# Performance work log

Hardware: AMD Instinct MI355X
Metric: run time of the kernel (lower is better)

Reference implementation:

```python
import jax, jax.numpy as jnp
import numpy as np

D = 192
HEADS = 4
HD = D // HEADS
R = 3  # correlation radius actually used in forward_level
NDISP = (2 * R + 1) ** 2  # 49
T = 3  # frames -> 2 consecutive pairs
ITERS = 4


def layer_norm(x, w, b, eps=1e-5):
    m = jnp.mean(x, axis=-1, keepdims=True)
    v = jnp.var(x, axis=-1, keepdims=True)
    return (x - m) / jnp.sqrt(v + eps) * w + b


def mha(x, in_w, in_b, out_w, out_b):
    # torch nn.MultiheadAttention, batch_first, self-attention
    B, N, _ = x.shape
    qkv = x @ in_w.T + in_b
    q, k, v = jnp.split(qkv, 3, axis=-1)
    q = q.reshape(B, N, HEADS, HD).transpose(0, 2, 1, 3) * (1.0 / float(np.sqrt(HD)))
    k = k.reshape(B, N, HEADS, HD).transpose(0, 2, 1, 3)
    v = v.reshape(B, N, HEADS, HD).transpose(0, 2, 1, 3)
    att = jax.nn.softmax(jnp.einsum('bhqd,bhkd->bhqk', q, k), axis=-1)
    y = jnp.einsum('bhqk,bhkd->bhqd', att, v).transpose(0, 2, 1, 3).reshape(B, N, D)
    return y @ out_w.T + out_b


def tblock(x, p):
    ln1w, ln1b, inw, inb, ow, ob, ln2w, ln2b, w1, b1, w2, b2 = p
    x = x + mha(layer_norm(x, ln1w, ln1b), inw, inb, ow, ob)
    h = layer_norm(x, ln2w, ln2b)
    h = jax.nn.gelu(h @ w1.T + b1, approximate=False) @ w2.T + b2
    return x + h


def local_corr(f1, f2):
    C = f1.shape[1]
    scale = 1.0 / float(np.sqrt(C))
    outs = []
    for dy in range(-R, R + 1):
        for dx in range(-R, R + 1):
            f2s = jnp.roll(f2, (dy, dx), axis=(2, 3))
            outs.append(jnp.sum(f1 * f2s, axis=1) * scale)
    return jnp.stack(outs, axis=1)


def grid_sample_bilinear_border(img, grid):
    # img: B,C,H,W; grid: B,Ho,Wo,2 with (x,y) in [-1,1]; align_corners=True, border padding
    B, C, H, W = img.shape
    x = jnp.clip((grid[..., 0] + 1.0) * 0.5 * (W - 1), 0.0, W - 1)
    y = jnp.clip((grid[..., 1] + 1.0) * 0.5 * (H - 1), 0.0, H - 1)
    x0 = jnp.floor(x); y0 = jnp.floor(y)
    x1 = jnp.minimum(x0 + 1, W - 1); y1 = jnp.minimum(y0 + 1, H - 1)
    wx = (x - x0)[:, None]; wy = (y - y0)[:, None]
    imgf = img.reshape(B, C, H * W)
    Ho, Wo = x.shape[1], x.shape[2]
    def gather(yy, xx):
        idx = (yy * W + xx).astype(jnp.int32).reshape(B, 1, Ho * Wo)
        return jnp.take_along_axis(imgf, idx, axis=2).reshape(B, C, Ho, Wo)
    v00 = gather(y0, x0); v01 = gather(y0, x1)
    v10 = gather(y1, x0); v11 = gather(y1, x1)
    return v00 * (1 - wx) * (1 - wy) + v01 * wx * (1 - wy) + v10 * (1 - wx) * wy + v11 * wx * wy


def warp(img, flow):
    # flow in pixels, Bx2xHxW
    B, C, H, W = img.shape
    xs = jnp.linspace(-1.0, 1.0, W); ys = jnp.linspace(-1.0, 1.0, H)
    gx, gy = jnp.meshgrid(xs, ys)  # each (H, W), 'xy' indexing
    base = jnp.stack([gx, gy], axis=-1)[None]
    off = jnp.stack([flow[:, 0] * (2.0 / max(W - 1, 1)),
                     flow[:, 1] * (2.0 / max(H - 1, 1))], axis=-1)
    return grid_sample_bilinear_border(img, base + off)


def upsample2x_align(img):
    # F.interpolate(scale_factor=2, mode='bilinear', align_corners=True)
    B, C, H, W = img.shape
    Ho, Wo = 2 * H, 2 * W
    xs = jnp.linspace(-1.0, 1.0, Wo); ys = jnp.linspace(-1.0, 1.0, Ho)
    gx, gy = jnp.meshgrid(xs, ys)
    grid = jnp.broadcast_to(jnp.stack([gx, gy], axis=-1)[None], (B, Ho, Wo, 2))
    return grid_sample_bilinear_border(img, grid)


def conv2d(x, w, b):
    y = jax.lax.conv_general_dilated(x, w, (1, 1), ((1, 1), (1, 1)),
                                     dimension_numbers=('NCHW', 'OIHW', 'NCHW'))
    return y + b[None, :, None, None]


def _forward(feats_l1, feats_l2, feats_l3, tok_w, tok_b,
             lcm_ln1_w, lcm_ln1_b, lcm_in_w, lcm_in_b, lcm_out_w, lcm_out_b,
             lcm_ln2_w, lcm_ln2_b, lcm_mlp_w1, lcm_mlp_b1, lcm_mlp_w2, lcm_mlp_b2,
             gtr_ln1_w, gtr_ln1_b, gtr_in_w, gtr_in_b, gtr_out_w, gtr_out_b,
             gtr_ln2_w, gtr_ln2_b, gtr_mlp_w1, gtr_mlp_b1, gtr_mlp_w2, gtr_mlp_b2,
             head_w1, head_b1, head_w2, head_b2,
             ref1_w1, ref1_b1, ref1_w2, ref1_b2,
             ref0_w1, ref0_b1, ref0_w2, ref0_b2):
    feats = [[feats_l1[t] for t in range(T)],
             [feats_l2[t] for t in range(T)],
             [feats_l3[t] for t in range(T)]]
    # ---- CostTokenizer ----
    tokens = []
    for lvl in range(3):
        toks = []
        for k in range(T - 1):
            corr = local_corr(feats[lvl][k], feats[lvl][k + 1])
            toks.append(jnp.einsum('bchw,dc->bdhw', corr, tok_w[lvl]) + tok_b[lvl][None, :, None, None])
        tokens.append(toks)
    lcm_p = [(lcm_ln1_w[i], lcm_ln1_b[i], lcm_in_w[i], lcm_in_b[i], lcm_out_w[i], lcm_out_b[i],
              lcm_ln2_w[i], lcm_ln2_b[i], lcm_mlp_w1[i], lcm_mlp_b1[i], lcm_mlp_w2[i], lcm_mlp_b2[i])
             for i in range(lcm_ln1_w.shape[0])]
    gtr_p = [(gtr_ln1_w[i], gtr_ln1_b[i], gtr_in_w[i], gtr_in_b[i], gtr_out_w[i], gtr_out_b[i],
              gtr_ln2_w[i], gtr_ln2_b[i], gtr_mlp_w1[i], gtr_mlp_b1[i], gtr_mlp_w2[i], gtr_mlp_b2[i])
             for i in range(gtr_ln1_w.shape[0])]
    # ---- LatentCostMemory (EMA state; .detach() -> stop_gradient; state resets when N changes) ----
    state = None
    latent = []
    for toks in tokens:
        lvl_lat = []
        for tok in toks:
            B_, Dd, H, W = tok.shape
            x = tok.reshape(B_, Dd, H * W).transpose(0, 2, 1)  # b (h w) d
            for p in lcm_p:
                x = tblock(x, p)
            if state is None or state.shape[1] != x.shape[1]:
                state = jax.lax.stop_gradient(x)
            x = 0.8 * x + 0.2 * state
            state = jax.lax.stop_gradient(x)
            lvl_lat.append(x.transpose(0, 2, 1))  # b d n
        latent.append(lvl_lat)
    H8, W8 = feats[1][0].shape[-2:]
    coarse = []
    for lat in latent[1]:
        x = lat.transpose(0, 2, 1)
        for p in gtr_p:
            x = tblock(x, p)
        fv = jax.nn.gelu(x @ head_w1.T + head_b1, approximate=False) @ head_w2.T + head_b2
        coarse.append(fv.transpose(0, 2, 1).reshape(-1, 2, H8, W8))
    # ---- MSRecurrentDecoder ----
    outs = []
    for k, f8 in enumerate(coarse):
        cur = f8
        for _ in range(ITERS):
            w10 = warp(feats[1][k + 1], cur)
            x = jnp.concatenate([feats[1][k], cur, w10], axis=1)
            cur = cur + conv2d(jax.nn.gelu(conv2d(x, ref1_w1, ref1_b1), approximate=False), ref1_w2, ref1_b2)
        cur2 = upsample2x_align(cur)
        for _ in range(ITERS):
            w10 = warp(feats[0][k + 1], cur2)
            x = jnp.concatenate([feats[0][k], cur2, w10], axis=1)
            cur2 = cur2 + conv2d(jax.nn.gelu(conv2d(x, ref0_w1, ref0_b1), approximate=False), ref0_w2, ref0_b2)
        outs.append(cur2)
    return jnp.stack(outs)  # [pairs, B, 2, H/4, W/4]


def setup_inputs():
    key = jax.random.key(0)
    ks = iter(jax.random.split(key, 64))
    def rn(shape, s=1.0):
        return jax.random.normal(next(ks), shape, dtype=jnp.float32) * s
    B = 1
    inp = {}
    inp['feats_l1'] = rn((T, B, 64, 64, 64))
    inp['feats_l2'] = rn((T, B, 128, 32, 32))
    inp['feats_l3'] = rn((T, B, 192, 16, 16))
    inp['tok_w'] = rn((3, D, NDISP), 0.02)
    inp['tok_b'] = rn((3, D), 0.02)
    for pre, n in (('lcm', 6), ('gtr', 2)):
        inp[pre + '_ln1_w'] = jnp.ones((n, D), jnp.float32)
        inp[pre + '_ln1_b'] = jnp.zeros((n, D), jnp.float32)
        inp[pre + '_in_w'] = rn((n, 3 * D, D), 0.02)
        inp[pre + '_in_b'] = rn((n, 3 * D), 0.02)
        inp[pre + '_out_w'] = rn((n, D, D), 0.02)
        inp[pre + '_out_b'] = rn((n, D), 0.02)
        inp[pre + '_ln2_w'] = jnp.ones((n, D), jnp.float32)
        inp[pre + '_ln2_b'] = jnp.zeros((n, D), jnp.float32)
        inp[pre + '_mlp_w1'] = rn((n, 4 * D, D), 0.02)
        inp[pre + '_mlp_b1'] = rn((n, 4 * D), 0.02)
        inp[pre + '_mlp_w2'] = rn((n, D, 4 * D), 0.02)
        inp[pre + '_mlp_b2'] = rn((n, D), 0.02)
    inp['head_w1'] = rn((D, D), 0.02); inp['head_b1'] = rn((D,), 0.02)
    inp['head_w2'] = rn((2, D), 0.02); inp['head_b2'] = rn((2,), 0.02)
    inp['ref1_w1'] = rn((128, 258, 3, 3), 0.02); inp['ref1_b1'] = rn((128,), 0.02)
    inp['ref1_w2'] = rn((2, 128, 3, 3), 0.02); inp['ref1_b2'] = rn((2,), 0.02)
    inp['ref0_w1'] = rn((64, 130, 3, 3), 0.02); inp['ref0_b1'] = rn((64,), 0.02)
    inp['ref0_w2'] = rn((2, 64, 3, 3), 0.02); inp['ref0_b2'] = rn((2,), 0.02)
    return inp


def reference(feats_l1, feats_l2, feats_l3, tok_w, tok_b,
              lcm_ln1_w, lcm_ln1_b, lcm_in_w, lcm_in_b, lcm_out_w, lcm_out_b,
              lcm_ln2_w, lcm_ln2_b, lcm_mlp_w1, lcm_mlp_b1, lcm_mlp_w2, lcm_mlp_b2,
              gtr_ln1_w, gtr_ln1_b, gtr_in_w, gtr_in_b, gtr_out_w, gtr_out_b,
              gtr_ln2_w, gtr_ln2_b, gtr_mlp_w1, gtr_mlp_b1, gtr_mlp_w2, gtr_mlp_b2,
              head_w1, head_b1, head_w2, head_b2,
              ref1_w1, ref1_b1, ref1_w2, ref1_b2,
              ref0_w1, ref0_b1, ref0_w2, ref0_b2):
    return _forward(feats_l1, feats_l2, feats_l3, tok_w, tok_b,
                    lcm_ln1_w, lcm_ln1_b, lcm_in_w, lcm_in_b, lcm_out_w, lcm_out_b,
                    lcm_ln2_w, lcm_ln2_b, lcm_mlp_w1, lcm_mlp_b1, lcm_mlp_w2, lcm_mlp_b2,
                    gtr_ln1_w, gtr_ln1_b, gtr_in_w, gtr_in_b, gtr_out_w, gtr_out_b,
                    gtr_ln2_w, gtr_ln2_b, gtr_mlp_w1, gtr_mlp_b1, gtr_mlp_w2, gtr_mlp_b2,
                    head_w1, head_b1, head_w2, head_b2,
                    ref1_w1, ref1_b1, ref1_w2, ref1_b2,
                    ref0_w1, ref0_b1, ref0_w2, ref0_b2)
```

## Files before the change

### kernel.cpp

```cpp
#include <hip/hip_runtime.h>
#include <hip/hip_bf16.h>

typedef __hip_bfloat16 bf16;
typedef short bf16x8 __attribute__((ext_vector_type(8)));
typedef float f32x4 __attribute__((ext_vector_type(4)));

#define DEV __device__ __forceinline__

DEV float bf2f(bf16 v) { return __bfloat162float(v); }
DEV bf16 f2bf(float v) { return __float2bfloat16(v); }
DEV unsigned short bfr(float f) {
  bf16 h = __float2bfloat16(f);
  return *reinterpret_cast<unsigned short*>(&h);
}
DEV float shf(unsigned short u) {
  unsigned int x = ((unsigned int)u) << 16;
  return *reinterpret_cast<float*>(&x);
}
DEV float gelu_exact(float x) { return 0.5f * x * (1.0f + erff(x * 0.70710678118654752f)); }

DEV float ldw(const void* p, long i, int isb) {
  return isb ? __bfloat162float(((const bf16*)p)[i]) : ((const float*)p)[i];
}

// ... 40 lines not shown
  if (i >= n) return;
  int s = i / (NP * ICP);
  int r = i - s * NP * ICP;
  int oc = r / ICP, icp = r - oc * ICP;
  float v = 0.0f;
  if (oc < OC) {
    int ic = -1;
    if (icp < C) ic = icp;
    else if (icp < 2 * C) ic = icp - C + C + 2;
    else if (icp < 2 * C + 2) ic = icp - 2 * C + C;
    if (ic >= 0 && ic < ICT) v = ldw(src, ((long)oc * ICT + ic) * 9 + s, isb);
  }
  dst[i] = f2bf(v);
}

__global__ void k_trans_feats(const void* __restrict__ in, bf16* __restrict__ Fp,
                              int F, int C, int HW, const int* __restrict__ fl) {
  int isb = *fl;
  int cpg = C >> 3;
  int n = F * HW * cpg;
  int i = blockIdx.x * blockDim.x + threadIdx.x;
  if (i >= n) return;
  int p = i % HW;
  int rem = i / HW;
  int c8 = rem % cpg;
  int f = rem / cpg;
  long base = (long)f * C * HW + (long)(c8 * 8) * HW + p;
  union { unsigned short u[8]; uint4 v; } pk;
#pragma unroll
  for (int j = 0; j < 8; ++j) pk.u[j] = bfr(ldw(in, base + (long)j * HW, isb));
  *(uint4*)((unsigned short*)Fp + ((long)f * HW + p) * C + c8 * 8) = pk.v;
}

__global__ void k_fill_feats(const bf16* __restrict__ Fp, bf16* __restrict__ Ap,
                             int C, int ICP, int H, int W) {
  int HW = H * W;
  int cpg = C >> 3;
  int n = 2 * HW * cpg;
  int i = blockIdx.x * blockDim.x + threadIdx.x;
  if (i >= n) return;
  int g = i % cpg;
  int rem = i / cpg;
  int p = rem % HW;
  int b = rem / HW;
  int h = p / W, w = p - h * W;
  const unsigned short* src = (const unsigned short*)Fp + ((long)b * HW + p) * C + g * 8;
  unsigned short* dst = (unsigned short*)Ap +
      ((long)b * (H + 2) * (W + 2) + (long)(h + 1) * (W + 2) + w + 1) * ICP + g * 8;
  *(uint4*)dst = *(const uint4*)src;
}

__global__ void k_warp_pack(const bf16* __restrict__ Fp, const float* __restrict__ flow,
                            bf16* __restrict__ Ap, int C, int ICP, int H, int W) {
  int HW = H * W;
  int cpg = C >> 3;
  int n = 2 * HW * cpg;
  int i = blockIdx.x * blockDim.x + threadIdx.x;
  if (i >= n) return;
  int g = i % cpg;
  int rem = i / cpg;
  int p = rem % HW;
  int b = rem / HW;
  int h = p / W, w = p - h * W;
  const float* fl = flow + (long)b * 2 * HW;
  float fx = fl[p], fy = fl[HW + p];
  unsigned short* drow = (unsigned short*)Ap +
      ((long)b * (H + 2) * (W + 2) + (long)(h + 1) * (W + 2) + w + 1) * ICP;
  if (g == 0) { drow[2 * C] = bfr(fx); drow[2 * C + 1] = bfr(fy); }
  float x = fminf(fmaxf((float)w + fx, 0.0f), (float)(W - 1));
  float y = fminf(fmaxf((float)h + fy, 0.0f), (float)(H - 1));
  int x0 = (int)floorf(x), y0 = (int)floorf(y);
  int x1 = min(x0 + 1, W - 1), y1 = min(y0 + 1, H - 1);
  float wx = x - (float)x0, wy = y - (float)y0;
  float w00 = (1 - wx) * (1 - wy), w01 = wx * (1 - wy);
  float w10 = (1 - wx) * wy, w11 = wx * wy;
  const unsigned short* f = (const unsigned short*)Fp + (long)(b + 1) * HW * C;
  int c = g * 8;
  union { unsigned short u[8]; uint4 v; } a = { .v = *(const uint4*)(f + (long)(y0 * W + x0) * C + c) };
  union { unsigned short u[8]; uint4 v; } bb = { .v = *(const uint4*)(f + (long)(y0 * W + x1) * C + c) };
  union { unsigned short u[8]; uint4 v; } cc = { .v = *(const uint4*)(f + (long)(y1 * W + x0) * C + c) };
  union { unsigned short u[8]; uint4 v; } dd = { .v = *(const uint4*)(f + (long)(y1 * W + x1) * C + c) };
  union { unsigned short u[8]; uint4 v; } o;
#pragma unroll
  for (int j = 0; j < 8; ++j) {
    float v = shf(a.u[j]) * w00 + shf(bb.u[j]) * w01 + shf(cc.u[j]) * w10 + shf(dd.u[j]) * w11;
    o.u[j] = bfr(v);
  }
  *(uint4*)(drow + C + c) = o.v;
}

template <int MW, int NT, int MODE>
__global__ __launch_bounds__(256) void k_conv_mfma(
    const bf16* __restrict__ Ap, int ICP, const bf16* __restrict__ Wp,
    const float* __restrict__ bias, const float* __restrict__ res,
    void* __restrict__ out, int NOUT, int H, int W, int lgW) {
  constexpr int NWN = 4 / MW;
  constexpr int BM = MW * 16;
  constexpr int BN = NWN * NT * 16;
  __shared__ unsigned short Asm[198][40];
  __shared__ unsigned short Wsm[9 * BN][40];
  int tid = threadIdx.x;
  int wv = tid >> 6, ln = tid & 63, quad = ln >> 4, l16 = ln & 15;
  int wm = wv % MW, wn = wv / MW;
  int n0 = blockIdx.x * BN;
  int m0 = blockIdx.y * BM;
  int b = blockIdx.z;
  int Wp2 = W + 2;
  int CW = (BM < W) ? BM : W;
  int lgCW = (CW == 64) ? 6 : 5;
  int RO = (BM > W) ? (BM >> lgW) : 1;
  int ACW = CW + 2;
  int AR = (RO + 2) * ACW;
  int py0 = m0 >> lgW;
  int px0 = m0 & (W - 1);
  const unsigned short* A = (const unsigned short*)Ap + (long)b * (H + 2) * Wp2 * ICP;
  int NPr = (MODE == 0) ? NOUT : 16;
  int nk = ICP >> 5;
  f32x4 acc[NT] = {};
  int mm_local = wm * 16 + l16;
  int plr = mm_local >> lgCW;
  int plc = mm_local & (CW - 1);
// ... 49 lines not shown
        ((float*)out)[(long)b * 2 * HW + (long)n * HW + mmo] = v;
      }
    }
  }
}

__global__ void k_corr(const bf16* __restrict__ Fp2, bf16* __restrict__ corrT) {
  __shared__ unsigned short f1r[128];
  int p = blockIdx.x;
  int b = blockIdx.y;
  int t = threadIdx.x;
  const unsigned short* f1 = (const unsigned short*)Fp2 + ((long)b * 1024 + p) * 128;
  if (t < 16) *(uint4*)&f1r[t * 8] = *(const uint4*)(f1 + t * 8);
  __syncthreads();
  long rowo = ((long)b * 1024 + p) * 64;
  if (t < 49) {
    int dy = t / 7 - 3, dx = t % 7 - 3;
    int h = p >> 5, w = p & 31;
    int p2 = (((h - dy) & 31) << 5) | ((w - dx) & 31);
    const unsigned short* f2 = (const unsigned short*)Fp2 + ((long)(b + 1) * 1024 + p2) * 128;
    float s = 0.0f;
    for (int c = 0; c < 128; c += 8) {
      union { unsigned short u[8]; uint4 v; } av = { .v = *(const uint4*)&f1r[c] };
      union { unsigned short u[8]; uint4 v; } bv = { .v = *(const uint4*)(f2 + c) };
#pragma unroll
      for (int j = 0; j < 8; ++j) s += shf(av.u[j]) * shf(bv.u[j]);
    }
    corrT[rowo + t] = f2bf(s * 0.08838834764831845f);
  } else {
    corrT[rowo + t] = f2bf(0.0f);
  }
}

template <int KT, int ACT, bool HASRES, int AMODE, int OUTBF, int VT>
__global__ __launch_bounds__(256) void k_gemm_mfma2(
    const void* __restrict__ A, const void* __restrict__ W, long woff,
    const void* __restrict__ bias, long boff, const int* __restrict__ flb,
    const float* __restrict__ res, void* __restrict__ C,
    int M, int N, const int* __restrict__ fl,
    const unsigned short* __restrict__ mop, const float* __restrict__ mml,
    bf16* __restrict__ vtout,
    const void* __restrict__ lnw, long lnwoff,
    const void* __restrict__ lnb, long lnboff) {
  (void)M;
  int isb = *fl;
  __shared__ unsigned short Asm[6][64][40];
  __shared__ unsigned short Wsm[6][64][40];
  int tid = threadIdx.x;
  int wv = tid >> 6, ln = tid & 63;
  int quad = ln >> 4, l16 = ln & 15;
  int m0 = blockIdx.y * 64, n0 = blockIdx.x * 64;
  f32x4 acc[4] = {};
  constexpr int NKC = ((KT < 192) ? KT : 192) >> 5;
  for (int s0 = 0; s0 < KT; s0 += 192) {
    if (s0) __syncthreads();
    for (int i = tid; i < NKC * 256; i += 256) {
      int c4 = i & 3, r = (i >> 2) & 63, kc = i >> 8;
      long eo = woff + (long)(n0 + r) * KT + s0 + kc * 32 + c4 * 8;
      if (isb) {
        *(uint4*)&Wsm[kc][r][c4 * 8] = *(const uint4*)((const unsigned short*)W + eo);
      } else {
        const float* wp = (const float*)W + eo;
        float4 w0 = *(const float4*)wp;
        float4 w1 = *(const float4*)(wp + 4);
        union { unsigned short u[8]; uint4 v; } pk;
        pk.u[0] = bfr(w0.x); pk.u[1] = bfr(w0.y); pk.u[2] = bfr(w0.z); pk.u[3] = bfr(w0.w);
        pk.u[4] = bfr(w1.x); pk.u[5] = bfr(w1.y); pk.u[6] = bfr(w1.z); pk.u[7] = bfr(w1.w);
        *(uint4*)&Wsm[kc][r][c4 * 8] = pk.v;
      }
    }
    if constexpr (AMODE == 1) {
      for (int i = tid; i < NKC * 256; i += 256) {
        int c4 = i & 3, r = (i >> 2) & 63, kc = i >> 8;
        const unsigned short* ap =
            (const unsigned short*)A + (long)(m0 + r) * KT + s0 + kc * 32 + c4 * 8;
        *(uint4*)&Asm[kc][r][c4 * 8] = *(const uint4*)ap;
      }
    } else if constexpr (AMODE == 0) {
      for (int i = tid; i < NKC * 256; i += 256) {
        int c4 = i & 3, r = (i >> 2) & 63, kc = i >> 8;
        const float* ap = (const float*)A + (long)(m0 + r) * KT + s0 + kc * 32 + c4 * 8;
        float4 a0 = *(const float4*)ap;
        float4 a1 = *(const float4*)(ap + 4);
        union { unsigned short u[8]; uint4 v; } pk;
        pk.u[0] = bfr(a0.x); pk.u[1] = bfr(a0.y); pk.u[2] = bfr(a0.z); pk.u[3] = bfr(a0.w);
        pk.u[4] = bfr(a1.x); pk.u[5] = bfr(a1.y); pk.u[6] = bfr(a1.z); pk.u[7] = bfr(a1.w);
        *(uint4*)&Asm[kc][r][c4 * 8] = pk.v;
      }
    } else if constexpr (AMODE == 3) {
      int row = tid >> 2, j = tid & 3;
      const float* xr = (const float*)A + (long)(m0 + row) * 192 + j * 8;
      float av[48];
#pragma unroll
      for (int kc = 0; kc < 6; ++kc) {
        float4 v0 = *(const float4*)(xr + kc * 32);
        float4 v1 = *(const float4*)(xr + kc * 32 + 4);
        av[kc * 8 + 0] = v0.x; av[kc * 8 + 1] = v0.y;
        av[kc * 8 + 2] = v0.z; av[kc * 8 + 3] = v0.w;
        av[kc * 8 + 4] = v1.x; av[kc * 8 + 5] = v1.y;
        av[kc * 8 + 6] = v1.z; av[kc * 8 + 7] = v1.w;
      }
      float sum = 0.0f;
#pragma unroll
      for (int q = 0; q < 48; ++q) sum += av[q];
      sum += __shfl_xor(sum, 1);
      sum += __shfl_xor(sum, 2);
      float mean = sum * (1.0f / 192.0f);
      float vs = 0.0f;
#pragma unroll
      for (int q = 0; q < 48; ++q) { float d = av[q] - mean; vs += d * d; }
      vs += __shfl_xor(vs, 1);
      vs += __shfl_xor(vs, 2);
      float rstd = rsqrtf(vs * (1.0f / 192.0f) + 1e-5f);
#pragma unroll
      for (int kc = 0; kc < 6; ++kc) {
        union { unsigned short u[8]; uint4 v; } pk;
#pragma unroll
        for (int e = 0; e < 8; ++e) {
          long k = kc * 32 + j * 8 + e;
          float g = ldw(lnw, lnwoff + k, isb);
          float bb = ldw(lnb, lnboff + k, isb);
          pk.u[e] = bfr((av[kc * 8 + e] - mean) * rstd * g + bb);
        }
        *(uint4*)&Asm[kc][row][j * 8] = pk.v;
      }
    } else {
      int row = tid >> 2, j = tid & 3;
      int m = m0 + row;
      int rr = m & 1023, bb = m >> 10;
#pragma unroll
      for (int kc = 0; kc < 6; ++kc) {
        int k = kc * 32 + j * 8;
        int h = k / 48;
        int d0 = k - h * 48;
        long idx[4];
        float ms[4], ls[4];
        float Ms = -1e30f;
#pragma unroll
        for (int s = 0; s < 4; ++s) {
          idx[s] = (((long)s * 2 + bb) * 4 + h) * 1024 + rr;
          ms[s] = mml[idx[s] * 2];
          ls[s] = mml[idx[s] * 2 + 1];
          Ms = fmaxf(Ms, ms[s]);
        }
        float e[4], L = 0.0f;
#pragma unroll
        for (int s = 0; s < 4; ++s) { e[s] = __expf(ms[s] - Ms); L += ls[s] * e[s]; }
        float invL = 1.0f / L;
        union { unsigned short u[8]; uint4 v; } pk;
#pragma unroll
        for (int e2 = 0; e2 < 8; ++e2) {
          float o = 0.0f;
#pragma unroll
          for (int s = 0; s < 4; ++s) o += shf(mop[idx[s] * 48 + d0 + e2]) * e[s];
          pk.u[e2] = bfr(o * invL);
        }
        *(uint4*)&Asm[kc][row][j * 8] = pk.v;
      }
    }
    __syncthreads();
#pragma unroll
    for (int kc = 0; kc < NKC; ++kc) {
      bf16x8 af = *(const bf16x8*)&Asm[kc][wv * 16 + l16][quad * 8];
#pragma unroll
      for (int nt = 0; nt < 4; ++nt) {
        bf16x8 wf = *(const bf16x8*)&Wsm[kc][nt * 16 + l16][quad * 8];
        acc[nt] = __builtin_amdgcn_mfma_f32_16x16x32_bf16(af, wf, acc[nt], 0, 0, 0);
      }
    }
  }
  int isbb = *flb;
#pragma unroll
  for (int nt = 0; nt < 4; ++nt) {
    int n = n0 + nt * 16 + l16;
    float bv = ldw(bias, boff + n, isbb);
#pragma unroll
    for (int r = 0; r < 4; ++r) {
      int m = m0 + wv * 16 + quad * 4 + r;
      float v = acc[nt][r] + bv;
      if (HASRES) v += res[(long)m * N + n];
      if (ACT == 1) v = gelu_exact(v);
      if (OUTBF) ((bf16*)C)[(long)m * N + n] = f2bf(v);
      else ((float*)C)[(long)m * N + n] = v;
      if (VT) {
        if (n >= 384) {
          int hh = (n - 384) / 48, dd = (n - 384) % 48;
          int row = m & 1023, bb = m >> 10;
          vtout[((long)(bb * 4 + hh) * 48 + dd) * 1024 + row] = f2bf(v);
        }
      }
    }
  }
}

template <int ACT, bool HASRES, int FLOW>
__global__ __launch_bounds__(256) void k_gemm(const float* __restrict__ A,
                                              const void* __restrict__ W, long woff,
                                              const void* __restrict__ bias, long boff,
                                              const float* __restrict__ res,
                                              float* __restrict__ C, int M, int N, int K, int Kw,
                                              const int* __restrict__ fl) {
  int isb = *fl;
  __shared__ float As[16][132];
  __shared__ float Ws[16][68];
  int tid = threadIdx.x;
  int tx = tid & 15, ty = tid >> 4;
  int m0 = blockIdx.y * 128, n0 = blockIdx.x * 64;
  float acc[8][4] = {};
  for (int k0 = 0; k0 < K; k0 += 16) {
#pragma unroll
    for (int i = 0; i < 2; ++i) {
      int idx4 = tid + i * 256;
      int mm = idx4 >> 2, kc = (idx4 & 3) * 4;
      float4 v = *(const float4*)(A + (long)(m0 + mm) * K + k0 + kc);
      As[kc][mm] = v.x; As[kc + 1][mm] = v.y; As[kc + 2][mm] = v.z; As[kc + 3][mm] = v.w;
    }
#pragma unroll
    for (int i = 0; i < 4; ++i) {
      int idx = tid + i * 256;
      int nn = idx >> 4, kk = idx & 15;
      int gn = n0 + nn, gk = k0 + kk;
      Ws[kk][nn] = (gn < N && gk < Kw) ? ldw(W, woff + (long)gn * Kw + gk, isb) : 0.0f;
    }
    __syncthreads();
#pragma unroll
    for (int kk = 0; kk < 16; ++kk) {
      float4 a0 = *(const float4*)&As[kk][ty * 8];
      float4 a1 = *(const float4*)&As[kk][ty * 8 + 4];
      float4 w4 = *(const float4*)&Ws[kk][tx * 4];
      float av[8] = {a0.x, a0.y, a0.z, a0.w, a1.x, a1.y, a1.z, a1.w};
      float wv[4] = {w4.x, w4.y, w4.z, w4.w};
#pragma unroll
      for (int i = 0; i < 8; ++i)
#pragma unroll
        for (int j = 0; j < 4; ++j) acc[i][j] += av[i] * wv[j];
    }
    __syncthreads();
  }
#pragma unroll
  for (int i = 0; i < 8; ++i) {
    int gm = m0 + ty * 8 + i;
#pragma unroll
    for (int j = 0; j < 4; ++j) {
      int gn = n0 + tx * 4 + j;
      if (gn >= N) continue;
      float v = acc[i][j] + ldw(bias, boff + gn, isb);
      if (HASRES) v += res[(long)gm * N + gn];
      if (ACT == 1) v = gelu_exact(v);
      if (FLOW) {
        int bb2 = gm >> 10, p = gm & 1023;
        C[((long)bb2 * 2 + gn) * 1024 + p] = v;
      } else {
        C[(long)gm * N + gn] = v;
      }
    }
  }
}

__global__ __launch_bounds__(256) void k_attn_mfma(const bf16* __restrict__ qkv,
                                                   const bf16* __restrict__ vt,
                                                   unsigned short* __restrict__ opart,
                                                   float* __restrict__ ml) {
  __shared__ unsigned short Qs[64][72];
  __shared__ unsigned short Ks[64][72];
  __shared__ unsigned short Vs[48][72];
  __shared__ unsigned short Ps[64][72];
  int tid = threadIdx.x;
  int wv = tid >> 6, ln = tid & 63, quad = ln >> 4, l16 = ln & 15;
  int h = blockIdx.y, b = blockIdx.z;
  int qt = blockIdx.x >> 2, s = blockIdx.x & 3;
  int q0 = qt * 64;
  const unsigned short* qp = (const unsigned short*)qkv + (long)b * 1024 * 576;
  const unsigned short* vp = (const unsigned short*)vt + ((long)(b * 4 + h) * 48) * 1024;
  for (int i = tid; i < 384; i += 256) {
    int r = i / 6, c = i % 6;
    *(uint4*)&Qs[r][c * 8] = *(const uint4*)(qp + (long)(q0 + r) * 576 + h * 48 + c * 8);
  }
  for (int i = tid; i < 128; i += 256) {
    int r = i >> 1, c = 6 + (i & 1);
    uint4 z = {0, 0, 0, 0};
    *(uint4*)&Qs[r][c * 8] = z;
  }
  float m[4] = {-1e30f, -1e30f, -1e30f, -1e30f};
  float l[4] = {0.0f, 0.0f, 0.0f, 0.0f};
  f32x4 accO[3] = {};
  const float SC = 0.14433756729740643f;
  for (int kc = s * 4; kc < s * 4 + 4; ++kc) {
    int k0 = kc * 64;
// ... 143 lines not shown
  (void)ws_size; (void)n_in; (void)in_sizes; (void)out_size;

  int* flag = (int*)d_ws;
  int* oneflag = (int*)d_ws + 2;
  float* wsf = (float*)d_ws;
  float* F2   = wsf + 16;
  float* rA   = F2 + 393216;
  float* rX   = rA + 786432;
  float* rT   = rX + 393216;
  float* rY   = rT + 393216;
  float* big  = rY + 393216;
  float* fv   = big + 1572864;
  float* cur  = fv + 4096;
  float* cur2 = cur + 4096;
  float* cb1a = cur2 + 16384;
  float* cb1b = cb1a + 128;
  float* cb0a = cb1b + 16;
  float* cb0b = cb0a + 64;
  bf16* wtok  = (bf16*)(cb0b + 16);
  float* wpk  = cb0b + 16 + 6144;
  bf16* w1p1 = (bf16*)wpk;
  bf16* w1p2 = (bf16*)(wpk + 165888);
  bf16* w0p1 = (bf16*)(wpk + 175104);
  bf16* w0p2 = (bf16*)(wpk + 221184);

  float* x = rX;
  bf16* corrTb = (bf16*)big;
  bf16* qkvbb  = (bf16*)big;
  bf16* vtb    = (bf16*)(big + 655360);
  bf16* hidb   = (bf16*)big;
  unsigned short* opart = (unsigned short*)rA;
  float* mlbuf = rY;
  float* headh = rT;
  bf16* A0p   = (bf16*)rA;
  bf16* A1p   = (bf16*)rX;
  bf16* mid0p = (bf16*)rT;
  bf16* mid1p = (bf16*)rY;
  bf16* Fp2   = (bf16*)(big + 851968);
  bf16* Fp1   = (bf16*)(big + 1048576);

  k_detect<<<1, 256, 0, stream>>>((const unsigned short*)feats_l1, flag);
  k_setone<<<1, 1, 0, stream>>>(oneflag);
  k_cvt<<<1, 256, 0, stream>>>(ref1_b1, cb1a, 128, flag);
  k_cvt<<<1, 256, 0, stream>>>(ref1_b2, cb1b, 2, flag);
  k_cvt<<<1, 256, 0, stream>>>(ref0_b1, cb0a, 64, flag);
  k_cvt<<<1, 256, 0, stream>>>(ref0_b2, cb0b, 2, flag);
  k_padtokw<<<48, 256, 0, stream>>>(tok_w, wtok, flag);
  k_packw<<<1296, 256, 0, stream>>>(ref1_w1, w1p1, 128, 128, 258, 128, 288, 331776, flag);
  k_packw<<<72, 256, 0, stream>>>(ref1_w2, w1p2, 2, 128, 128, 16, 128, 18432, flag);
  k_packw<<<360, 256, 0, stream>>>(ref0_w1, w0p1, 64, 64, 130, 64, 160, 92160, flag);
  k_packw<<<36, 256, 0, stream>>>(ref0_w2, w0p2, 2, 64, 64, 16, 64, 9216, flag);
  k_trans_feats<<<192, 256, 0, stream>>>(feats_l2, Fp2, 3, 128, 1024, flag);
  k_trans_feats<<<384, 256, 0, stream>>>(feats_l1, Fp1, 3, 64, 4096, flag);

  k_corr<<<dim3(1024, 2), 64, 0, stream>>>(Fp2, corrTb);
  k_gemm_mfma2<64, 0, false, 1, 0, 0><<<dim3(3, 32), 256, 0, stream>>>(
      corrTb, wtok, 0, tok_b, 192, flag, nullptr, x, 2048, 192, oneflag,
      nullptr, nullptr, nullptr, nullptr, 0, nullptr, 0);

  auto run_block = [&](const void* ln1w, long o1, const void* ln1b, long o2,
                       const void* inw, long o3, const void* inb, long o4,
                       const void* ow, long o5, const void* ob, long o6,
                       const void* ln2w, long o7, const void* ln2b, long o8,
                       const void* w1, long o9, const void* b1, long o10,
                       const void* w2, long o11, const void* b2, long o12) {
    k_gemm_mfma2<192, 0, false, 3, 1, 1><<<dim3(9, 32), 256, 0, stream>>>(
        x, inw, o3, inb, o4, flag, nullptr, qkvbb, 2048, 576, flag,
        nullptr, nullptr, vtb, ln1w, o1, ln1b, o2);
    k_attn_mfma<<<dim3(64, 4, 2), 256, 0, stream>>>(qkvbb, vtb, opart, mlbuf);
    k_gemm_mfma2<192, 0, true, 2, 0, 0><<<dim3(3, 32), 256, 0, stream>>>(
        nullptr, ow, o5, ob, o6, flag, x, x, 2048, 192, flag,
        opart, mlbuf, nullptr, nullptr, 0, nullptr, 0);
    k_gemm_mfma2<192, 1, false, 3, 1, 0><<<dim3(12, 32), 256, 0, stream>>>(
        x, w1, o9, b1, o10, flag, nullptr, hidb, 2048, 768, flag,
        nullptr, nullptr, nullptr, ln2w, o7, ln2b, o8);
    k_gemm_mfma2<768, 0, true, 1, 0, 0><<<dim3(3, 32), 256, 0, stream>>>(
        hidb, w2, o11, b2, o12, flag, x, x, 2048, 192, flag,
        nullptr, nullptr, nullptr, nullptr, 0, nullptr, 0);
  };

  for (int i = 0; i < 6; ++i) {
    run_block(lcm_ln1_w, (long)i * 192, lcm_ln1_b, (long)i * 192,
              lcm_in_w, (long)i * 110592, lcm_in_b, (long)i * 576,
              lcm_out_w, (long)i * 36864, lcm_out_b, (long)i * 192,
              lcm_ln2_w, (long)i * 192, lcm_ln2_b, (long)i * 192,
              lcm_mlp_w1, (long)i * 147456, lcm_mlp_b1, (long)i * 768,
              lcm_mlp_w2, (long)i * 147456, lcm_mlp_b2, (long)i * 192);
  }
  k_ema<<<768, 256, 0, stream>>>(x);

  for (int i = 0; i < 2; ++i) {
    run_block(gtr_ln1_w, (long)i * 192, gtr_ln1_b, (long)i * 192,
              gtr_in_w, (long)i * 110592, gtr_in_b, (long)i * 576,
              gtr_out_w, (long)i * 36864, gtr_out_b, (long)i * 192,
              gtr_ln2_w, (long)i * 192, gtr_ln2_b, (long)i * 192,
              gtr_mlp_w1, (long)i * 147456, gtr_mlp_b1, (long)i * 768,
              gtr_mlp_w2, (long)i * 147456, gtr_mlp_b2, (long)i * 192);
  }

  k_gemm_mfma2<192, 1, false, 0, 0, 0><<<dim3(3, 32), 256, 0, stream>>>(
      x, head_w1, 0, head_b1, 0, flag, nullptr, headh, 2048, 192, flag,
      nullptr, nullptr, nullptr, nullptr, 0, nullptr, 0);
  k_gemm<0, false, 1><<<dim3(1, 16), 256, 0, stream>>>(headh, head_w2, 0, head_b2, 0, nullptr,
                                                       cur, 2048, 2, 192, 192, flag);

  k_zerosh<<<1920, 256, 0, stream>>>((unsigned short*)rA, 491520);
  k_fill_feats<<<128, 256, 0, stream>>>(Fp2, A1p, 128, 288, 32, 32);

  for (int it = 0; it < 4; ++it) {
    k_warp_pack<<<128, 256, 0, stream>>>(Fp2, cur, A1p, 128, 288, 32, 32);
    k_conv_mfma<2, 2, 0><<<dim3(2, 32, 2), 256, 0, stream>>>(
        A1p, 288, w1p1, cb1a, nullptr, mid1p, 128, 32, 32, 5);
    k_conv_mfma<4, 1, 1><<<dim3(1, 16, 2), 256, 0, stream>>>(
        mid1p, 128, w1p2, cb1b, cur, cur, 2, 32, 32, 5);
  }
  k_upsample<<<64, 256, 0, stream>>>(cur, cur2);
  k_fill_feats<<<256, 256, 0, stream>>>(Fp1, A0p, 64, 160, 64, 64);

  for (int it = 0; it < 4; ++it) {
    k_warp_pack<<<256, 256, 0, stream>>>(Fp1, cur2, A0p, 64, 160, 64, 64);
    k_conv_mfma<2, 2, 0><<<dim3(1, 128, 2), 256, 0, stream>>>(
        A0p, 160, w0p1, cb0a, nullptr, mid0p, 64, 64, 64, 6);
    k_conv_mfma<4, 1, 1><<<dim3(1, 64, 2), 256, 0, stream>>>(
        mid0p, 64, w0p2, cb0b, cur2, cur2, 2, 64, 64, 6);
  }

  k_out<<<64, 256, 0, stream>>>(cur2, d_out, flag);
}
```

Before: 1.087 ms.

## Fuse flow warp and feature packing into first refine conv; tune GEMM tiles

Introduces k_conv_warp, which builds the padded conv input tile in shared memory straight from the features and flow. It does the bilinear warp inline, so the separate fill and warp_pack kernels, their padded staging buffers and most of the zero-fill go away. The MFMA GEMM gains a BM template parameter, and the N=192 GEMMs use 32-row tiles to double the block count. The tiny head projection is moved from a scalar tiled GEMM to a wave-per-output reduction kernel. In exchange, warp work is recomputed for halo pixels and for each output-channel block, and the smaller GEMM tiles reuse weights less.

```diff
diff --git a/kernel.cpp b/kernel.cpp
--- a/kernel.cpp
+++ b/kernel.cpp
@@ -96,61 +96,113 @@
   *(uint4*)((unsigned short*)Fp + ((long)f * HW + p) * C + c8 * 8) = pk.v;
 }
 
-__global__ void k_fill_feats(const bf16* __restrict__ Fp, bf16* __restrict__ Ap,
-                             int C, int ICP, int H, int W) {
+template <int MW, int NT>
+__global__ __launch_bounds__(256) void k_conv_warp(
+    const bf16* __restrict__ Fp, const float* __restrict__ flow, int C, int ICP,
+    const bf16* __restrict__ Wp, const float* __restrict__ bias,
+    void* __restrict__ out, int NOUT, int H, int W, int lgW) {
+  constexpr int NWN = 4 / MW;
+  constexpr int BM = MW * 16;
+  constexpr int BN = NWN * NT * 16;
+  __shared__ unsigned short Asm[102][40];
+  __shared__ unsigned short Wsm[9 * BN][40];
+  int tid = threadIdx.x;
+  int wv = tid >> 6, ln = tid & 63, quad = ln >> 4, l16 = ln & 15;
+  int wm = wv % MW, wn = wv / MW;
+  int n0 = blockIdx.x * BN;
+  int m0 = blockIdx.y * BM;
+  int b = blockIdx.z;
   int HW = H * W;
-  int cpg = C >> 3;
-  int n = 2 * HW * cpg;
-  int i = blockIdx.x * blockDim.x + threadIdx.x;
-  if (i >= n) return;
-  int g = i % cpg;
-  int rem = i / cpg;
-  int p = rem % HW;
-  int b = rem / HW;
-  int h = p / W, w = p - h * W;
-  const unsigned short* src = (const unsigned short*)Fp + ((long)b * HW + p) * C + g * 8;
-  unsigned short* dst = (unsigned short*)Ap +
-      ((long)b * (H + 2) * (W + 2) + (long)(h + 1) * (W + 2) + w + 1) * ICP + g * 8;
-  *(uint4*)dst = *(const uint4*)src;
-}
-
-__global__ void k_warp_pack(const bf16* __restrict__ Fp, const float* __restrict__ flow,
-                            bf16* __restrict__ Ap, int C, int ICP, int H, int W) {
-  int HW = H * W;
-  int cpg = C >> 3;
-  int n = 2 * HW * cpg;
-  int i = blockIdx.x * blockDim.x + threadIdx.x;
-  if (i >= n) return;
-  int g = i % cpg;
-  int rem = i / cpg;
-  int p = rem % HW;
-  int b = rem / HW;
-  int h = p / W, w = p - h * W;
+  int CW = (BM < W) ? BM : W;
+  int lgCW = (CW == 64) ? 6 : 5;
+  int RO = (BM > W) ? (BM >> lgW) : 1;
+  int ACW = CW + 2;
+  int AR = (RO + 2) * ACW;
+  int py0 = m0 >> lgW;
+  int px0 = m0 & (W - 1);
+  const unsigned short* fcur = (const unsigned short*)Fp + (long)b * HW * C;
+  const unsigned short* fnxt = (const unsigned short*)Fp + (long)(b + 1) * HW * C;
   const float* fl = flow + (long)b * 2 * HW;
-  float fx = fl[p], fy = fl[HW + p];
-  unsigned short* drow = (unsigned short*)Ap +
-      ((long)b * (H + 2) * (W + 2) + (long)(h + 1) * (W + 2) + w + 1) * ICP;
-  if (g == 0) { drow[2 * C] = bfr(fx); drow[2 * C + 1] = bfr(fy); }
-  float x = fminf(fmaxf((float)w + fx, 0.0f), (float)(W - 1));
-  float y = fminf(fmaxf((float)h + fy, 0.0f), (float)(H - 1));
-  int x0 = (int)floorf(x), y0 = (int)floorf(y);
-  int x1 = min(x0 + 1, W - 1), y1 = min(y0 + 1, H - 1);
-  float wx = x - (float)x0, wy = y - (float)y0;
-  float w00 = (1 - wx) * (1 - wy), w01 = wx * (1 - wy);
-  float w10 = (1 - wx) * wy, w11 = wx * wy;
-  const unsigned short* f = (const unsigned short*)Fp + (long)(b + 1) * HW * C;
-  int c = g * 8;
-  union { unsigned short u[8]; uint4 v; } a = { .v = *(const uint4*)(f + (long)(y0 * W + x0) * C + c) };
-  union { unsigned short u[8]; uint4 v; } bb = { .v = *(const uint4*)(f + (long)(y0 * W + x1) * C + c) };
-  union { unsigned short u[8]; uint4 v; } cc = { .v = *(const uint4*)(f + (long)(y1 * W + x0) * C + c) };
-  union { unsigned short u[8]; uint4 v; } dd = { .v = *(const uint4*)(f + (long)(y1 * W + x1) * C + c) };
-  union { unsigned short u[8]; uint4 v; } o;
-#pragma unroll
-  for (int j = 0; j < 8; ++j) {
-    float v = shf(a.u[j]) * w00 + shf(bb.u[j]) * w01 + shf(cc.u[j]) * w10 + shf(dd.u[j]) * w11;
-    o.u[j] = bfr(v);
-  }
-  *(uint4*)(drow + C + c) = o.v;
+  int nk = ICP >> 5;
+  f32x4 acc[NT] = {};
+  int mm_local = wm * 16 + l16;
+  int plr = mm_local >> lgCW;
+  int plc = mm_local & (CW - 1);
+  for (int kc = 0; kc < nk; ++kc) {
+    int chbase = kc * 32;
+    for (int i = tid; i < AR * 4; i += 256) {
+      int r = i >> 2, c4 = i & 3;
+      int sr = r / ACW, sc = r - sr * ACW;
+      int py = py0 + sr - 1, px = px0 + sc - 1;
+      uint4 val = {0, 0, 0, 0};
+      if (py >= 0 && py < H && px >= 0 && px < W) {
+        int p = py * W + px;
+        int ch = chbase + c4 * 8;
+        if (ch < C) {
+          val = *(const uint4*)(fcur + (long)p * C + ch);
+        } else if (ch < 2 * C) {
+          float fx = fl[p], fy = fl[HW + p];
+          float x = fminf(fmaxf((float)px + fx, 0.0f), (float)(W - 1));
+          float y = fminf(fmaxf((float)py + fy, 0.0f), (float)(H - 1));
+          int x0 = (int)floorf(x), y0 = (int)floorf(y);
+          int x1 = min(x0 + 1, W - 1), y1 = min(y0 + 1, H - 1);
+          float wx = x - (float)x0, wy = y - (float)y0;
+          float w00 = (1 - wx) * (1 - wy), w01 = wx * (1 - wy);
+          float w10 = (1 - wx) * wy, w11 = wx * wy;
+          int c = ch - C;
+          union { unsigned short u[8]; uint4 v; } a = { .v = *(const uint4*)(fnxt + (long)(y0 * W + x0) * C + c) };
+          union { unsigned short u[8]; uint4 v; } bb = { .v = *(const uint4*)(fnxt + (long)(y0 * W + x1) * C + c) };
+          union { unsigned short u[8]; uint4 v; } cc = { .v = *(const uint4*)(fnxt + (long)(y1 * W + x0) * C + c) };
+          union { unsigned short u[8]; uint4 v; } dd = { .v = *(const uint4*)(fnxt + (long)(y1 * W + x1) * C + c) };
+          union { unsigned short u[8]; uint4 v; } o;
+#pragma unroll
+          for (int j = 0; j < 8; ++j) {
+            float v = shf(a.u[j]) * w00 + shf(bb.u[j]) * w01 + shf(cc.u[j]) * w10 + shf(dd.u[j]) * w11;
+            o.u[j] = bfr(v);
+          }
+          val = o.v;
+        } else if (ch == 2 * C) {
+          union { unsigned short u[8]; uint4 v; } o = { .v = {0, 0, 0, 0} };
+          o.u[0] = bfr(fl[p]);
+          o.u[1] = bfr(fl[HW + p]);
+          val = o.v;
+        }
+      }
+      *(uint4*)&Asm[r][c4 * 8] = val;
+    }
+    for (int i = tid; i < 9 * BN * 4; i += 256) {
+      int r = i >> 2, c4 = i & 3;
+      int s = r / BN, nl = r - s * BN;
+      long g = ((long)s * NOUT + n0 + nl) * ICP + kc * 32 + c4 * 8;
+      *(uint4*)&Wsm[r][c4 * 8] = *(const uint4*)((const unsigned short*)Wp + g);
+    }
+    __syncthreads();
+#pragma unroll
+    for (int s = 0; s < 9; ++s) {
+      int ky = s / 3, kx = s - ky * 3;
+      bf16x8 af = *(const bf16x8*)&Asm[(plr + ky) * ACW + plc + kx][quad * 8];
+#pragma unroll
+      for (int nt = 0; nt < NT; ++nt) {
+        bf16x8 wf = *(const bf16x8*)&Wsm[s * BN + (wn * NT + nt) * 16 + l16][quad * 8];
+        acc[nt] = __builtin_amdgcn_mfma_f32_16x16x32_bf16(af, wf, acc[nt], 0, 0, 0);
+      }
+    }
+    __syncthreads();
+  }
+  int Wp2 = W + 2;
+#pragma unroll
+  for (int nt = 0; nt < NT; ++nt) {
+    int n = n0 + (wn * NT + nt) * 16 + l16;
+    float bv = bias[n];
+#pragma unroll
+    for (int r = 0; r < 4; ++r) {
+      int mmo = m0 + wm * 16 + quad * 4 + r;
+      int py = mmo >> lgW, px = mmo & (W - 1);
+      float v = gelu_exact(acc[nt][r] + bv);
+      ((unsigned short*)out)[((long)b * (H + 2) * Wp2 + (long)(py + 1) * Wp2 + px + 1) * NOUT + n]
+          = bfr(v);
+    }
+  }
 }
 
 template <int MW, int NT, int MODE>
@@ -266,7 +318,7 @@
   }
 }
 
-template <int KT, int ACT, bool HASRES, int AMODE, int OUTBF, int VT>
+template <int KT, int BM, int ACT, bool HASRES, int AMODE, int OUTBF, int VT>
 __global__ __launch_bounds__(256) void k_gemm_mfma2(
     const void* __restrict__ A, const void* __restrict__ W, long woff,
     const void* __restrict__ bias, long boff, const int* __restrict__ flb,
@@ -278,14 +330,19 @@
     const void* __restrict__ lnb, long lnboff) {
   (void)M;
   int isb = *fl;
-  __shared__ unsigned short Asm[6][64][40];
-  __shared__ unsigned short Wsm[6][64][40];
+  constexpr int NKC = ((KT < 192) ? KT : 192) >> 5;
+  constexpr int WM = (BM == 64) ? 4 : 2;
+  constexpr int NTW = (BM == 64) ? 4 : 2;
+  constexpr int LPR = 256 / BM;
+  constexpr int EPL = 192 / LPR;
+  __shared__ unsigned short Asm[NKC][BM][40];
+  __shared__ unsigned short Wsm[NKC][64][40];
   int tid = threadIdx.x;
   int wv = tid >> 6, ln = tid & 63;
   int quad = ln >> 4, l16 = ln & 15;
-  int m0 = blockIdx.y * 64, n0 = blockIdx.x * 64;
-  f32x4 acc[4] = {};
-  constexpr int NKC = ((KT < 192) ? KT : 192) >> 5;
+  int wm = wv % WM, wn = wv / WM;
+  int m0 = blockIdx.y * BM, n0 = blockIdx.x * 64;
+  f32x4 acc[NTW] = {};
   for (int s0 = 0; s0 < KT; s0 += 192) {
     if (s0) __syncthreads();
     for (int i = tid; i < NKC * 256; i += 256) {
@@ -304,15 +361,15 @@
       }
     }
     if constexpr (AMODE == 1) {
-      for (int i = tid; i < NKC * 256; i += 256) {
-        int c4 = i & 3, r = (i >> 2) & 63, kc = i >> 8;
+      for (int i = tid; i < NKC * BM * 4; i += 256) {
+        int c4 = i & 3, r = (i >> 2) % BM, kc = i / (BM * 4);
         const unsigned short* ap =
             (const unsigned short*)A + (long)(m0 + r) * KT + s0 + kc * 32 + c4 * 8;
         *(uint4*)&Asm[kc][r][c4 * 8] = *(const uint4*)ap;
       }
     } else if constexpr (AMODE == 0) {
-      for (int i = tid; i < NKC * 256; i += 256) {
-        int c4 = i & 3, r = (i >> 2) & 63, kc = i >> 8;
+      for (int i = tid; i < NKC * BM * 4; i += 256) {
+        int c4 = i & 3, r = (i >> 2) % BM, kc = i / (BM * 4);
         const float* ap = (const float*)A + (long)(m0 + r) * KT + s0 + kc * 32 + c4 * 8;
         float4 a0 = *(const float4*)ap;
         float4 a1 = *(const float4*)(ap + 4);
@@ -322,49 +379,46 @@
         *(uint4*)&Asm[kc][r][c4 * 8] = pk.v;
       }
     } else if constexpr (AMODE == 3) {
-      int row = tid >> 2, j = tid & 3;
-      const float* xr = (const float*)A + (long)(m0 + row) * 192 + j * 8;
-      float av[48];
-#pragma unroll
-      for (int kc = 0; kc < 6; ++kc) {
-        float4 v0 = *(const float4*)(xr + kc * 32);
-        float4 v1 = *(const float4*)(xr + kc * 32 + 4);
-        av[kc * 8 + 0] = v0.x; av[kc * 8 + 1] = v0.y;
-        av[kc * 8 + 2] = v0.z; av[kc * 8 + 3] = v0.w;
-        av[kc * 8 + 4] = v1.x; av[kc * 8 + 5] = v1.y;
-        av[kc * 8 + 6] = v1.z; av[kc * 8 + 7] = v1.w;
+      int row = tid / LPR, j = tid % LPR;
+      const float* xr = (const float*)A + (long)(m0 + row) * 192 + j * EPL;
+      float av[EPL];
+#pragma unroll
+      for (int q4 = 0; q4 < EPL / 4; ++q4) {
+        float4 v = *(const float4*)(xr + q4 * 4);
+        av[q4 * 4 + 0] = v.x; av[q4 * 4 + 1] = v.y;
+        av[q4 * 4 + 2] = v.z; av[q4 * 4 + 3] = v.w;
       }
       float sum = 0.0f;
 #pragma unroll
-      for (int q = 0; q < 48; ++q) sum += av[q];
-      sum += __shfl_xor(sum, 1);
-      sum += __shfl_xor(sum, 2);
+      for (int q = 0; q < EPL; ++q) sum += av[q];
+#pragma unroll
+      for (int o = 1; o < LPR; o <<= 1) sum += __shfl_xor(sum, o);
       float mean = sum * (1.0f / 192.0f);
       float vs = 0.0f;
 #pragma unroll
-      for (int q = 0; q < 48; ++q) { float d = av[q] - mean; vs += d * d; }
-      vs += __shfl_xor(vs, 1);
-      vs += __shfl_xor(vs, 2);
+      for (int q = 0; q < EPL; ++q) { float d = av[q] - mean; vs += d * d; }
+#pragma unroll
+      for (int o = 1; o < LPR; o <<= 1) vs += __shfl_xor(vs, o);
       float rstd = rsqrtf(vs * (1.0f / 192.0f) + 1e-5f);
 #pragma unroll
-      for (int kc = 0; kc < 6; ++kc) {
+      for (int g = 0; g < EPL / 8; ++g) {
+        int k = j * EPL + g * 8;
         union { unsigned short u[8]; uint4 v; } pk;
 #pragma unroll
         for (int e = 0; e < 8; ++e) {
-          long k = kc * 32 + j * 8 + e;
-          float g = ldw(lnw, lnwoff + k, isb);
-          float bb = ldw(lnb, lnboff + k, isb);
-          pk.u[e] = bfr((av[kc * 8 + e] - mean) * rstd * g + bb);
+          float gg = ldw(lnw, lnwoff + k + e, isb);
+          float bb = ldw(lnb, lnboff + k + e, isb);
+          pk.u[e] = bfr((av[g * 8 + e] - mean) * rstd * gg + bb);
         }
-        *(uint4*)&Asm[kc][row][j * 8] = pk.v;
+        *(uint4*)&Asm[k >> 5][row][k & 31] = pk.v;
       }
     } else {
-      int row = tid >> 2, j = tid & 3;
+      int row = tid / LPR, j = tid % LPR;
       int m = m0 + row;
       int rr = m & 1023, bb = m >> 10;
 #pragma unroll
-      for (int kc = 0; kc < 6; ++kc) {
-        int k = kc * 32 + j * 8;
+      for (int g = 0; g < EPL / 8; ++g) {
+        int k = j * EPL + g * 8;
         int h = k / 48;
         int d0 = k - h * 48;
         long idx[4];
@@ -389,34 +443,34 @@
           for (int s = 0; s < 4; ++s) o += shf(mop[idx[s] * 48 + d0 + e2]) * e[s];
           pk.u[e2] = bfr(o * invL);
         }
-        *(uint4*)&Asm[kc][row][j * 8] = pk.v;
+        *(uint4*)&Asm[k >> 5][row][k & 31] = pk.v;
       }
     }
     __syncthreads();
 #pragma unroll
     for (int kc = 0; kc < NKC; ++kc) {
-      bf16x8 af = *(const bf16x8*)&Asm[kc][wv * 16 + l16][quad * 8];
-#pragma unroll
-      for (int nt = 0; nt < 4; ++nt) {
-        bf16x8 wf = *(const bf16x8*)&Wsm[kc][nt * 16 + l16][quad * 8];
+      bf16x8 af = *(const bf16x8*)&Asm[kc][wm * 16 + l16][quad * 8];
+#pragma unroll
+      for (int nt = 0; nt < NTW; ++nt) {
+        bf16x8 wf = *(const bf16x8*)&Wsm[kc][(wn * NTW + nt) * 16 + l16][quad * 8];
         acc[nt] = __builtin_amdgcn_mfma_f32_16x16x32_bf16(af, wf, acc[nt], 0, 0, 0);
       }
     }
   }
   int isbb = *flb;
 #pragma unroll
-  for (int nt = 0; nt < 4; ++nt) {
-    int n = n0 + nt * 16 + l16;
+  for (int nt = 0; nt < NTW; ++nt) {
+    int n = n0 + (wn * NTW + nt) * 16 + l16;
     float bv = ldw(bias, boff + n, isbb);
 #pragma unroll
     for (int r = 0; r < 4; ++r) {
-      int m = m0 + wv * 16 + quad * 4 + r;
+      int m = m0 + wm * 16 + quad * 4 + r;
       float v = acc[nt][r] + bv;
       if (HASRES) v += res[(long)m * N + n];
       if (ACT == 1) v = gelu_exact(v);
       if (OUTBF) ((bf16*)C)[(long)m * N + n] = f2bf(v);
       else ((float*)C)[(long)m * N + n] = v;
-      if (VT) {
+      if constexpr (VT) {
         if (n >= 384) {
           int hh = (n - 384) / 48, dd = (n - 384) % 48;
           int row = m & 1023, bb = m >> 10;
@@ -427,67 +481,26 @@
   }
 }
 
-template <int ACT, bool HASRES, int FLOW>
-__global__ __launch_bounds__(256) void k_gemm(const float* __restrict__ A,
-                                              const void* __restrict__ W, long woff,
-                                              const void* __restrict__ bias, long boff,
-                                              const float* __restrict__ res,
-                                              float* __restrict__ C, int M, int N, int K, int Kw,
-                                              const int* __restrict__ fl) {
+__global__ __launch_bounds__(256) void k_head2(const float* __restrict__ A,
+                                               const void* __restrict__ W,
+                                               const void* __restrict__ bias,
+                                               float* __restrict__ C,
+                                               const int* __restrict__ fl) {
   int isb = *fl;
-  __shared__ float As[16][132];
-  __shared__ float Ws[16][68];
-  int tid = threadIdx.x;
-  int tx = tid & 15, ty = tid >> 4;
-  int m0 = blockIdx.y * 128, n0 = blockIdx.x * 64;
-  float acc[8][4] = {};
-  for (int k0 = 0; k0 < K; k0 += 16) {
-#pragma unroll
-    for (int i = 0; i < 2; ++i) {
-      int idx4 = tid + i * 256;
-      int mm = idx4 >> 2, kc = (idx4 & 3) * 4;
-      float4 v = *(const float4*)(A + (long)(m0 + mm) * K + k0 + kc);
-      As[kc][mm] = v.x; As[kc + 1][mm] = v.y; As[kc + 2][mm] = v.z; As[kc + 3][mm] = v.w;
-    }
-#pragma unroll
-    for (int i = 0; i < 4; ++i) {
-      int idx = tid + i * 256;
-      int nn = idx >> 4, kk = idx & 15;
-      int gn = n0 + nn, gk = k0 + kk;
-      Ws[kk][nn] = (gn < N && gk < Kw) ? ldw(W, woff + (long)gn * Kw + gk, isb) : 0.0f;
-    }
-    __syncthreads();
-#pragma unroll
-    for (int kk = 0; kk < 16; ++kk) {
-      float4 a0 = *(const float4*)&As[kk][ty * 8];
-      float4 a1 = *(const float4*)&As[kk][ty * 8 + 4];
-      float4 w4 = *(const float4*)&Ws[kk][tx * 4];
-      float av[8] = {a0.x, a0.y, a0.z, a0.w, a1.x, a1.y, a1.z, a1.w};
-      float wv[4] = {w4.x, w4.y, w4.z, w4.w};
-#pragma unroll
-      for (int i = 0; i < 8; ++i)
-#pragma unroll
-        for (int j = 0; j < 4; ++j) acc[i][j] += av[i] * wv[j];
-    }
-    __syncthreads();
-  }
-#pragma unroll
-  for (int i = 0; i < 8; ++i) {
-    int gm = m0 + ty * 8 + i;
-#pragma unroll
-    for (int j = 0; j < 4; ++j) {
-      int gn = n0 + tx * 4 + j;
-      if (gn >= N) continue;
-      float v = acc[i][j] + ldw(bias, boff + gn, isb);
-      if (HASRES) v += res[(long)gm * N + gn];
-      if (ACT == 1) v = gelu_exact(v);
-      if (FLOW) {
-        int bb2 = gm >> 10, p = gm & 1023;
-        C[((long)bb2 * 2 + gn) * 1024 + p] = v;
-      } else {
-        C[(long)gm * N + gn] = v;
-      }
-    }
+  int wv = threadIdx.x >> 6, ln = threadIdx.x & 63;
+  int gw = blockIdx.x * 4 + wv;
+  int m = gw >> 1, n = gw & 1;
+  const float* a = A + (long)m * 192;
+  float s = 0.0f;
+#pragma unroll
+  for (int q = 0; q < 3; ++q) {
+    int j = ln + q * 64;
+    s += a[j] * ldw(W, (long)n * 192 + j, isb);
+  }
+  for (int o = 32; o; o >>= 1) s += __shfl_xor(s, o);
+  if (ln == 0) {
+    int b = m >> 10, p = m & 1023;
+    C[((long)b * 2 + n) * 1024 + p] = s + ldw(bias, n, isb);
   }
 }
 
@@ -697,8 +710,6 @@
   unsigned short* opart = (unsigned short*)rA;
   float* mlbuf = rY;
   float* headh = rT;
-  bf16* A0p   = (bf16*)rA;
-  bf16* A1p   = (bf16*)rX;
   bf16* mid0p = (bf16*)rT;
   bf16* mid1p = (bf16*)rY;
   bf16* Fp2   = (bf16*)(big + 851968);
@@ -719,7 +730,7 @@
   k_trans_feats<<<384, 256, 0, stream>>>(feats_l1, Fp1, 3, 64, 4096, flag);
 
   k_corr<<<dim3(1024, 2), 64, 0, stream>>>(Fp2, corrTb);
-  k_gemm_mfma2<64, 0, false, 1, 0, 0><<<dim3(3, 32), 256, 0, stream>>>(
+  k_gemm_mfma2<64, 32, 0, false, 1, 0, 0><<<dim3(3, 64), 256, 0, stream>>>(
       corrTb, wtok, 0, tok_b, 192, flag, nullptr, x, 2048, 192, oneflag,
       nullptr, nullptr, nullptr, nullptr, 0, nullptr, 0);
 
@@ -729,17 +740,17 @@
                        const void* ln2w, long o7, const void* ln2b, long o8,
                        const void* w1, long o9, const void* b1, long o10,
                        const void* w2, long o11, const void* b2, long o12) {
-    k_gemm_mfma2<192, 0, false, 3, 1, 1><<<dim3(9, 32), 256, 0, stream>>>(
+    k_gemm_mfma2<192, 64, 0, false, 3, 1, 1><<<dim3(9, 32), 256, 0, stream>>>(
         x, inw, o3, inb, o4, flag, nullptr, qkvbb, 2048, 576, flag,
         nullptr, nullptr, vtb, ln1w, o1, ln1b, o2);
     k_attn_mfma<<<dim3(64, 4, 2), 256, 0, stream>>>(qkvbb, vtb, opart, mlbuf);
-    k_gemm_mfma2<192, 0, true, 2, 0, 0><<<dim3(3, 32), 256, 0, stream>>>(
+    k_gemm_mfma2<192, 32, 0, true, 2, 0, 0><<<dim3(3, 64), 256, 0, stream>>>(
         nullptr, ow, o5, ob, o6, flag, x, x, 2048, 192, flag,
         opart, mlbuf, nullptr, nullptr, 0, nullptr, 0);
-    k_gemm_mfma2<192, 1, false, 3, 1, 0><<<dim3(12, 32), 256, 0, stream>>>(
+    k_gemm_mfma2<192, 64, 1, false, 3, 1, 0><<<dim3(12, 32), 256, 0, stream>>>(
         x, w1, o9, b1, o10, flag, nullptr, hidb, 2048, 768, flag,
         nullptr, nullptr, nullptr, ln2w, o7, ln2b, o8);
-    k_gemm_mfma2<768, 0, true, 1, 0, 0><<<dim3(3, 32), 256, 0, stream>>>(
+    k_gemm_mfma2<768, 32, 0, true, 1, 0, 0><<<dim3(3, 64), 256, 0, stream>>>(
         hidb, w2, o11, b2, o12, flag, x, x, 2048, 192, flag,
         nullptr, nullptr, nullptr, nullptr, 0, nullptr, 0);
   };
@@ -763,29 +774,24 @@
               gtr_mlp_w2, (long)i * 147456, gtr_mlp_b2, (long)i * 192);
   }
 
-  k_gemm_mfma2<192, 1, false, 0, 0, 0><<<dim3(3, 32), 256, 0, stream>>>(
+  k_gemm_mfma2<192, 32, 1, false, 0, 0, 0><<<dim3(3, 64), 256, 0, stream>>>(
       x, head_w1, 0, head_b1, 0, flag, nullptr, headh, 2048, 192, flag,
       nullptr, nullptr, nullptr, nullptr, 0, nullptr, 0);
-  k_gemm<0, false, 1><<<dim3(1, 16), 256, 0, stream>>>(headh, head_w2, 0, head_b2, 0, nullptr,
-                                                       cur, 2048, 2, 192, 192, flag);
-
-  k_zerosh<<<1920, 256, 0, stream>>>((unsigned short*)rA, 491520);
-  k_fill_feats<<<128, 256, 0, stream>>>(Fp2, A1p, 128, 288, 32, 32);
+  k_head2<<<1024, 256, 0, stream>>>(headh, head_w2, head_b2, cur, flag);
+
+  k_zerosh<<<768, 256, 0, stream>>>((unsigned short*)rT, 196608);
 
   for (int it = 0; it < 4; ++it) {
-    k_warp_pack<<<128, 256, 0, stream>>>(Fp2, cur, A1p, 128, 288, 32, 32);
-    k_conv_mfma<2, 2, 0><<<dim3(2, 32, 2), 256, 0, stream>>>(
-        A1p, 288, w1p1, cb1a, nullptr, mid1p, 128, 32, 32, 5);
+    k_conv_warp<2, 2><<<dim3(2, 32, 2), 256, 0, stream>>>(
+        Fp2, cur, 128, 288, w1p1, cb1a, mid1p, 128, 32, 32, 5);
     k_conv_mfma<4, 1, 1><<<dim3(1, 16, 2), 256, 0, stream>>>(
         mid1p, 128, w1p2, cb1b, cur, cur, 2, 32, 32, 5);
   }
   k_upsample<<<64, 256, 0, stream>>>(cur, cur2);
-  k_fill_feats<<<256, 256, 0, stream>>>(Fp1, A0p, 64, 160, 64, 64);
 
   for (int it = 0; it < 4; ++it) {
-    k_warp_pack<<<256, 256, 0, stream>>>(Fp1, cur2, A0p, 64, 160, 64, 64);
-    k_conv_mfma<2, 2, 0><<<dim3(1, 128, 2), 256, 0, stream>>>(
-        A0p, 160, w0p1, cb0a, nullptr, mid0p, 64, 64, 64, 6);
+    k_conv_warp<2, 2><<<dim3(1, 128, 2), 256, 0, stream>>>(
+        Fp1, cur2, 64, 160, w0p1, cb0a, mid0p, 64, 64, 64, 6);
     k_conv_mfma<4, 1, 1><<<dim3(1, 64, 2), 256, 0, stream>>>(
         mid0p, 64, w0p2, cb0b, cur2, cur2, 2, 64, 64, 6);
   }
```

Result: faster. 1.029 ms (-5.3%).
